# Performance work log

Hardware: AMD Instinct MI355X
Metric: run time of the kernel (lower is better)

Reference implementation:

```python
import jax, jax.numpy as jnp
import numpy as np
import math

BS, N_AGENTS, TOPK = 256, 64, 8
IN_DIM, HID, ATT, N_ACT = 128, 256, 64, 16


def setup_inputs() -> dict:
    key = jax.random.key(0)
    ks = jax.random.split(key, 20)
    s = 0.05
    return {
        "inputs": jax.random.normal(ks[0], (BS * N_AGENTS, IN_DIM), jnp.float32),
        "hidden_state": jax.random.normal(ks[1], (BS * N_AGENTS, HID), jnp.float32),
        "msg": jax.random.normal(ks[2], (BS * N_AGENTS, HID), jnp.float32),
        "topk_indices": jax.random.randint(ks[3], (BS, N_AGENTS, TOPK), 0, N_AGENTS, jnp.int32),
        "fc1_w": jax.random.normal(ks[4], (HID, IN_DIM), jnp.float32) * s,
        "fc1_b": jnp.zeros((HID,), jnp.float32),
        "gru_w_ih": jax.random.normal(ks[5], (3 * HID, HID), jnp.float32) * s,
        "gru_b_ih": jnp.zeros((3 * HID,), jnp.float32),
        "gru_w_hh": jax.random.normal(ks[6], (3 * HID, HID), jnp.float32) * s,
        "gru_b_hh": jnp.zeros((3 * HID,), jnp.float32),
        "q_w": jax.random.normal(ks[7], (ATT, HID), jnp.float32) * s,
        "q_b": jnp.zeros((ATT,), jnp.float32),
        "k_w": jax.random.normal(ks[8], (ATT, HID), jnp.float32) * s,
        "k_b": jnp.zeros((ATT,), jnp.float32),
        "v_w": jax.random.normal(ks[9], (HID, HID), jnp.float32) * s,
        "v_b": jnp.zeros((HID,), jnp.float32),
        "fc2a_w": jax.random.normal(ks[10], (HID, 2 * HID), jnp.float32) * s,
        "fc2a_b": jnp.zeros((HID,), jnp.float32),
        "fc2b_w": jax.random.normal(ks[11], (N_ACT, HID), jnp.float32) * s,
        "fc2b_b": jnp.zeros((N_ACT,), jnp.float32),
    }


def _forward(inputs, hidden_state, msg, topk_indices,
             fc1_w, fc1_b, gru_w_ih, gru_b_ih, gru_w_hh, gru_b_hh,
             q_w, q_b, k_w, k_b, v_w, v_b, fc2a_w, fc2a_b, fc2b_w, fc2b_b):
    # fc1 + ReLU
    x = jax.nn.relu(inputs @ fc1_w.T + fc1_b)  # [B*N, HID]
    # GRUCell (torch semantics)
    gi = x @ gru_w_ih.T + gru_b_ih             # [B*N, 3H]
    gh = hidden_state @ gru_w_hh.T + gru_b_hh
    i_r, i_z, i_n = jnp.split(gi, 3, axis=-1)
    h_r, h_z, h_n = jnp.split(gh, 3, axis=-1)
    r = jax.nn.sigmoid(i_r + h_r)
    z = jax.nn.sigmoid(i_z + h_z)
    n = jnp.tanh(i_n + r * h_n)
    h = (1.0 - z) * n + z * hidden_state       # [B*N, HID]

    # communicate: gather top-k neighbor messages, attend, aggregate
    msg_r = msg.reshape(BS, N_AGENTS, HID)
    msg_received = jax.vmap(lambda m, idx: m[idx])(msg_r, topk_indices)  # [B,N,K,HID]
    ego_h = h.reshape(BS, N_AGENTS, HID)
    q = ego_h @ q_w.T + q_b                    # [B,N,ATT]
    k = msg_received @ k_w.T + k_b             # [B,N,K,ATT]
    logits = jnp.einsum('bnka,bna->bnk', k, q) / math.sqrt(ATT)
    attn = jax.nn.softmax(logits, axis=-1)     # [B,N,K]
    m = msg_received @ v_w.T + v_b             # [B,N,K,HID]
    m_agg = jnp.einsum('bnk,bnkh->bnh', attn, m).reshape(BS * N_AGENTS, HID)

    out = jnp.concatenate([h, m_agg], axis=-1)  # [B*N, 2H]
    q_out = jax.nn.relu(out @ fc2a_w.T + fc2a_b) @ fc2b_w.T + fc2b_b  # [B*N, N_ACT]
    return q_out, h, m_agg


def reference(inputs, hidden_state, msg, topk_indices,
              fc1_w, fc1_b, gru_w_ih, gru_b_ih, gru_w_hh, gru_b_hh,
              q_w, q_b, k_w, k_b, v_w, v_b, fc2a_w, fc2a_b, fc2b_w, fc2b_b):
    return _forward(inputs, hidden_state, msg, topk_indices,
                    fc1_w, fc1_b, gru_w_ih, gru_b_ih, gru_w_hh, gru_b_hh,
                    q_w, q_b, k_w, k_b, v_w, v_b, fc2a_w, fc2a_b, fc2b_w, fc2b_b)
```

## Files before the change

kernel.cpp:

```cpp
#include <hip/hip_runtime.h>

typedef __bf16 bf16;
typedef __attribute__((ext_vector_type(8))) __bf16 bf16x8;
typedef __attribute__((ext_vector_type(4))) __bf16 bf16x4;
typedef __attribute__((ext_vector_type(4))) float f32x4;

static constexpr int ROWS = 16384;

static constexpr size_t OFF_WFC1 = 0;
static constexpr size_t OFF_WRX  = 32768;
static constexpr size_t OFF_WZX  = 98304;
static constexpr size_t OFF_WNI  = 163840;
static constexpr size_t OFF_WRH  = 229376;
static constexpr size_t OFF_WZH  = 294912;
static constexpr size_t OFF_WNH  = 360448;
static constexpr size_t OFF_WQ   = 425984;
static constexpr size_t OFF_WKV  = 442368;
static constexpr size_t OFF_F2AH = 524288;
static constexpr size_t OFF_F2AM = 589824;
static constexpr size_t OFF_WF2B = 655360;
static constexpr size_t OFF_INSW = 659456;

struct SwzSeg { const float* src; bf16* dst; int items; int k8s; int k32; int ld; };
struct SwzArgs { SwzSeg seg[14]; int count; };

__global__ __launch_bounds__(256) void swz_k(SwzArgs a) {
    const int tid = blockIdx.x * 256 + threadIdx.x;
    const int stride = gridDim.x * 256;
    for (int s = 0; s < a.count; ++s) {
        const float* __restrict__ src = a.seg[s].src;
        bf16* __restrict__ dst = a.seg[s].dst;
        const int items = a.seg[s].items, k8s = a.seg[s].k8s;
        const int k32c = a.seg[s].k32, ld = a.seg[s].ld;
        for (int i = tid; i < items; i += stride) {
            const int n = i >> k8s, kb = i & ((1 << k8s) - 1);
            const int k0 = kb << 3;
            const int lane = (n & 15) | ((kb & 3) << 4);
            const size_t off = ((size_t)((n >> 4) * k32c + (kb >> 2)) * 64 + lane) * 8;
            const float* p = src + (size_t)n * ld + k0;
            float4 f0 = *(const float4*)p;
            float4 f1 = *(const float4*)(p + 4);
            bf16x8 o = { (bf16)f0.x, (bf16)f0.y, (bf16)f0.z, (bf16)f0.w,
                         (bf16)f1.x, (bf16)f1.y, (bf16)f1.z, (bf16)f1.w };
            *(bf16x8*)(dst + off) = o;
        }
    }
}

template<int FM, int FN, int K32>
__device__ __forceinline__ void mm_swz(f32x4 (&acc)[FM][FN],
    const bf16* __restrict__ sA, int lda,
    const bf16* __restrict__ W, int lane)
{
    const int lr = lane & 15, lk = (lane >> 4) << 3;
    #pragma unroll
    for (int k32 = 0; k32 < K32; ++k32) {
        bf16x8 a[FM], b[FN];
        #pragma unroll
        for (int j = 0; j < FN; ++j)
            b[j] = *(const bf16x8*)(W + ((size_t)(j * K32 + k32) * 64 + lane) * 8);
        #pragma unroll
        for (int i = 0; i < FM; ++i)
            a[i] = *(const bf16x8*)&sA[(i * 16 + lr) * lda + k32 * 32 + lk];
        #pragma unroll
        for (int i = 0; i < FM; ++i)
            #pragma unroll
            for (int j = 0; j < FN; ++j)
                acc[i][j] = __builtin_amdgcn_mfma_f32_16x16x32_bf16(a[i], b[j], acc[i][j], 0, 0, 0);
    }
}

template<int FM, int FN, int K32>
__device__ __forceinline__ void mm_gg(f32x4 (&acc)[FM][FN],
    const bf16* __restrict__ A, const bf16* __restrict__ W, int lane)
{
    #pragma unroll
    for (int k32 = 0; k32 < K32; ++k32) {
        bf16x8 a[FM], b[FN];
        #pragma unroll
        for (int i = 0; i < FM; ++i)
            a[i] = *(const bf16x8*)(A + ((size_t)(i * K32 + k32) * 64 + lane) * 8);
        #pragma unroll
        for (int j = 0; j < FN; ++j)
            b[j] = *(const bf16x8*)(W + ((size_t)(j * K32 + k32) * 64 + lane) * 8);
        #pragma unroll
        for (int i = 0; i < FM; ++i)
            #pragma unroll
            for (int j = 0; j < FN; ++j)
                acc[i][j] = __builtin_amdgcn_mfma_f32_16x16x32_bf16(a[i], b[j], acc[i][j], 0, 0, 0);
    }
}

__device__ __forceinline__ float sigmf(float x) { return 1.f / (1.f + __expf(-x)); }
__device__ __forceinline__ float tanh_fast(float x) {
    x = fminf(fmaxf(x, -15.f), 15.f);
    float e2 = __expf(2.f * x);
    return (e2 - 1.f) / (e2 + 1.f);
}

__global__ __launch_bounds__(1024)
void mega_k(const bf16* __restrict__ insw, const float* __restrict__ hid_f,
            const float* __restrict__ msg_f, const int* __restrict__ topk,
            const bf16* __restrict__ Wfc1, const float* __restrict__ fc1_b,
            const bf16* __restrict__ WrX, const bf16* __restrict__ WrH,
            const bf16* __restrict__ WzX, const bf16* __restrict__ WzH,
            const bf16* __restrict__ Wni, const bf16* __restrict__ Wnh,
            const float* __restrict__ b_ih, const float* __restrict__ b_hh,
            const bf16* __restrict__ Wq, const float* __restrict__ q_b,
            const bf16* __restrict__ Wkv, const float* __restrict__ v_bias,
            const bf16* __restrict__ f2aH, const bf16* __restrict__ f2aM,
            const float* __restrict__ f2a_b,
            const bf16* __restrict__ Wf2b, const float* __restrict__ f2b_b,
            float* __restrict__ h_out, float* __restrict__ magg_out,
            float* __restrict__ q_out)
{
    __shared__ bf16 sH[64 * 264];
    __shared__ bf16 sB[64 * 264];
    __shared__ bf16 sG[64 * 264];
    __shared__ bf16 sM[64 * 264];
    __shared__ bf16 sQ[64 * 72];
    __shared__ bf16 sK[64 * 72];
    __shared__ int  sIdx[512];
    const int tid = threadIdx.x;
    const int wave = tid >> 6, lane = tid & 63;
    const int b64 = blockIdx.x * 64;
    const int lr = lane & 15, l4 = (lane >> 4) << 2, lk = (lane >> 4) << 3;

    #pragma unroll
    for (int c = tid; c < 4096; c += 1024) {
        int r = c >> 6, cg = (c & 63) << 2;
        float4 f = *(const float4*)(hid_f + (size_t)(b64 + r) * 256 + cg);
        float4 g = *(const float4*)(msg_f + (size_t)(b64 + r) * 256 + cg);
        bf16x4 oh = { (bf16)f.x, (bf16)f.y, (bf16)f.z, (bf16)f.w };
        bf16x4 og = { (bf16)g.x, (bf16)g.y, (bf16)g.z, (bf16)g.w };
        *(bf16x4*)&sH[r * 264 + cg] = oh;
        *(bf16x4*)&sG[r * 264 + cg] = og;
    }
    if (tid < 512) sIdx[tid] = topk[(size_t)blockIdx.x * 512 + tid];

    {
        f32x4 fa[1][4] = {};
        mm_gg<1, 4, 4>(fa, insw + (size_t)(blockIdx.x * 4 + (wave & 3)) * 4 * 512,
                       Wfc1 + (size_t)((wave >> 2) * 4) * 4 * 512, lane);
        #pragma unroll
        for (int j = 0; j < 4; ++j) {
            const int col = (wave >> 2) * 64 + j * 16 + lr;
            const float bv = fc1_b[col];
            #pragma unroll
            for (int rr = 0; rr < 4; ++rr)
                sB[((wave & 3) * 16 + l4 + rr) * 264 + col] = (bf16)fmaxf(fa[0][j][rr] + bv, 0.f);
        }
    }
    __syncthreads();

    f32x4 rg[4] = {}, zg[4] = {}, ng[4] = {}, hg[4] = {};
    {
        const size_t nb = (size_t)wave * 8 * 512;
        const bf16 *pRX = WrX + nb, *pZX = WzX + nb, *pNI = Wni + nb;
        const bf16 *pRH = WrH + nb, *pZH = WzH + nb, *pNH = Wnh + nb;
        #pragma unroll
        for (int k32 = 0; k32 < 8; ++k32) {
            const size_t bo = (size_t)k32 * 512 + lane * 8;
            bf16x8 brx = *(const bf16x8*)(pRX + bo);
            bf16x8 bzx = *(const bf16x8*)(pZX + bo);
            bf16x8 bni = *(const bf16x8*)(pNI + bo);
            bf16x8 brh = *(const bf16x8*)(pRH + bo);
            bf16x8 bzh = *(const bf16x8*)(pZH + bo);
            bf16x8 bnh = *(const bf16x8*)(pNH + bo);
            __builtin_amdgcn_s_setprio(1);
            #pragma unroll
            for (int i = 0; i < 4; ++i) {
                bf16x8 ax = *(const bf16x8*)&sB[(i * 16 + lr) * 264 + k32 * 32 + lk];
                rg[i] = __builtin_amdgcn_mfma_f32_16x16x32_bf16(ax, brx, rg[i], 0, 0, 0);
                zg[i] = __builtin_amdgcn_mfma_f32_16x16x32_bf16(ax, bzx, zg[i], 0, 0, 0);
                ng[i] = __builtin_amdgcn_mfma_f32_16x16x32_bf16(ax, bni, ng[i], 0, 0, 0);
            }
            #pragma unroll
            for (int i = 0; i < 4; ++i) {
                bf16x8 ah = *(const bf16x8*)&sH[(i * 16 + lr) * 264 + k32 * 32 + lk];
                rg[i] = __builtin_amdgcn_mfma_f32_16x16x32_bf16(ah, brh, rg[i], 0, 0, 0);
                zg[i] = __builtin_amdgcn_mfma_f32_16x16x32_bf16(ah, bzh, zg[i], 0, 0, 0);
                hg[i] = __builtin_amdgcn_mfma_f32_16x16x32_bf16(ah, bnh, hg[i], 0, 0, 0);
            }
            __builtin_amdgcn_s_setprio(0);
        }
    }
    {
        const int col = wave * 16 + lr;
        const float br = b_ih[col] + b_hh[col];
        const float bz = b_ih[256 + col] + b_hh[256 + col];
        const float bi = b_ih[512 + col], bh = b_hh[512 + col];
        #pragma unroll
        for (int i = 0; i < 4; ++i)
            #pragma unroll
            for (int rr = 0; rr < 4; ++rr) {
                const int row = i * 16 + l4 + rr;
                const float rv = sigmf(rg[i][rr] + br);
                const float zv = sigmf(zg[i][rr] + bz);
                const float nn = tanh_fast((ng[i][rr] + bi) + rv * (hg[i][rr] + bh));
                const float hd = (float)sH[row * 264 + col];
                const float h = (1.f - zv) * nn + zv * hd;
                sM[row * 264 + col] = (bf16)h;
            }
    }
    __syncthreads();

    if (wave < 4) {
        f32x4 a[4][2] = {};
        mm_swz<4, 2, 8>(a, sG, 264, Wkv + (size_t)(wave * 2) * 8 * 512, lane);
        #pragma unroll
        for (int i = 0; i < 4; ++i)
            #pragma unroll
            for (int j = 0; j < 2; ++j) {
                const int col = (wave * 2 + j) * 16 + lr;
                #pragma unroll
                for (int rr = 0; rr < 4; ++rr) {
                    const int row = i * 16 + l4 + rr;
                    if (col < 64) sK[row * 72 + col] = (bf16)a[i][j][rr];
                    else          sB[row * 264 + col - 64] = (bf16)a[i][j][rr];
                }
            }
    } else {
        f32x4 a[4][1] = {};
        mm_swz<4, 1, 8>(a, sG, 264, Wkv + (size_t)(4 + wave) * 8 * 512, lane);
        const int col = (4 + wave) * 16 + lr;
        #pragma unroll
        for (int i = 0; i < 4; ++i)
            #pragma unroll
            for (int rr = 0; rr < 4; ++rr)
                sB[(i * 16 + l4 + rr) * 264 + col - 64] = (bf16)a[i][0][rr];
    }
    {
        f32x4 qa[1][1] = {};
        mm_swz<1, 1, 8>(qa, sM + (wave & 3) * 16 * 264, 264,
                        Wq + (size_t)(wave >> 2) * 8 * 512, lane);
        const int col = (wave >> 2) * 16 + lr;
        const float bv = q_b[col];
        #pragma unroll
        for (int rr = 0; rr < 4; ++rr)
            sQ[((wave & 3) * 16 + l4 + rr) * 72 + col] = (bf16)(qa[0][0][rr] + bv);
    }
    #pragma unroll
    for (int u = 0; u < 4; ++u) {
        int c = tid + u * 1024;
        int r = c >> 6, cg = (c & 63) << 2;
        bf16x4 hv = *(const bf16x4*)&sM[r * 264 + cg];
        float4 o = { (float)hv[0], (float)hv[1], (float)hv[2], (float)hv[3] };
        *(float4*)(h_out + (size_t)(b64 + r) * 256 + cg) = o;
    }
    __syncthreads();

    const int kk = lane >> 3, dg = lane & 7;
    #pragma unroll
    for (int uu = 0; uu < 4; ++uu) {
        const int u = wave * 4 + uu;
        const int rowk = sIdx[u * 8 + kk];
        bf16x8 q8 = *(const bf16x8*)&sQ[u * 72 + dg * 8];
        bf16x8 k8 = *(const bf16x8*)&sK[rowk * 72 + dg * 8];
        float s = 0.f;
        #pragma unroll
        for (int t = 0; t < 8; ++t) s += (float)q8[t] * (float)k8[t];
        s += __shfl_xor(s, 1); s += __shfl_xor(s, 2); s += __shfl_xor(s, 4);
        float logit = s * 0.125f;
        float mx = logit;
        mx = fmaxf(mx, __shfl_xor(mx, 8));
        mx = fmaxf(mx, __shfl_xor(mx, 16));
        mx = fmaxf(mx, __shfl_xor(mx, 32));
        float e = __expf(logit - mx);
        float den = e;
        den += __shfl_xor(den, 8); den += __shfl_xor(den, 16); den += __shfl_xor(den, 32);
        const float wv = e / den;
        float a0 = 0.f, a1 = 0.f, a2 = 0.f, a3 = 0.f;
        #pragma unroll
        for (int k = 0; k < 8; ++k) {
            float wk = __shfl(wv, k * 8);
            int   rk = __shfl(rowk, k * 8);
            bf16x4 v = *(const bf16x4*)&sB[rk * 264 + lane * 4];
            a0 += wk * (float)v[0]; a1 += wk * (float)v[1];
            a2 += wk * (float)v[2]; a3 += wk * (float)v[3];
        }
        float4 vb = *(const float4*)(v_bias + lane * 4);
        a0 += vb.x; a1 += vb.y; a2 += vb.z; a3 += vb.w;
        float4 res = { a0, a1, a2, a3 };
        *(float4*)(magg_out + (size_t)(b64 + u) * 256 + lane * 4) = res;
        bf16x4 rb = { (bf16)a0, (bf16)a1, (bf16)a2, (bf16)a3 };
        *(bf16x4*)&sH[u * 264 + lane * 4] = rb;
    }
    __syncthreads();

    {
        const size_t nb = (size_t)wave * 8 * 512;
        f32x4 ya[4] = {};
        const bf16* pH = f2aH + nb;
        const bf16* pM = f2aM + nb;
        const int lo = lane * 8;
        bf16x8 cH = *(const bf16x8*)(pH + lo);
        bf16x8 cM = *(const bf16x8*)(pM + lo);
        #pragma unroll
        for (int k = 0; k < 8; ++k) {
            bf16x8 nH, nM;
            if (k < 7) {
                nH = *(const bf16x8*)(pH + (k + 1) * 512 + lo);
                nM = *(const bf16x8*)(pM + (k + 1) * 512 + lo);
            }
            __builtin_amdgcn_s_setprio(1);
            #pragma unroll
            for (int i = 0; i < 4; ++i) {
                bf16x8 aH = *(const bf16x8*)&sM[(i * 16 + lr) * 264 + k * 32 + lk];
                ya[i] = __builtin_amdgcn_mfma_f32_16x16x32_bf16(aH, cH, ya[i], 0, 0, 0);
            }
            #pragma unroll
            for (int i = 0; i < 4; ++i) {
                bf16x8 aM = *(const bf16x8*)&sH[(i * 16 + lr) * 264 + k * 32 + lk];
                ya[i] = __builtin_amdgcn_mfma_f32_16x16x32_bf16(aM, cM, ya[i], 0, 0, 0);
            }
            __builtin_amdgcn_s_setprio(0);
            cH = nH; cM = nM;
        }
        const int col = wave * 16 + lr;
        const float bv = f2a_b[col];
        #pragma unroll
        for (int i = 0; i < 4; ++i)
            #pragma unroll
            for (int rr = 0; rr < 4; ++rr)
                sG[(i * 16 + l4 + rr) * 264 + col] = (bf16)fmaxf(ya[i][rr] + bv, 0.f);
    }
    __syncthreads();

    if (wave < 4) {
        f32x4 acc[1][1] = {};
        mm_swz<1, 1, 8>(acc, sG + wave * 16 * 264, 264, Wf2b, lane);
        const float bv = f2b_b[lr];
        #pragma unroll
        for (int rr = 0; rr < 4; ++rr)
            q_out[(size_t)(b64 + wave * 16 + l4 + rr) * 16 + lr] = acc[0][0][rr] + bv;
    }
}

extern "C" void kernel_launch(void* const* d_in, const int* in_sizes, int n_in,
                              void* d_out, int out_size, void* d_ws, size_t ws_size,
                              hipStream_t stream)
{
    const float* in_f   = (const float*)d_in[0];
    const float* hid_f  = (const float*)d_in[1];
    const float* msg_f  = (const float*)d_in[2];
    const int*   topk   = (const int*)d_in[3];
    const float* fc1w_f = (const float*)d_in[4];
    const float* fc1_b  = (const float*)d_in[5];
    const float* wih_f  = (const float*)d_in[6];
    const float* b_ih   = (const float*)d_in[7];
    const float* whh_f  = (const float*)d_in[8];
    const float* b_hh   = (const float*)d_in[9];
    const float* qw_f   = (const float*)d_in[10];
    const float* q_b    = (const float*)d_in[11];
    const float* kw_f   = (const float*)d_in[12];
    const float* vw_f   = (const float*)d_in[14];
    const float* v_b    = (const float*)d_in[15];
    const float* f2aw_f = (const float*)d_in[16];
    const float* f2a_b  = (const float*)d_in[17];
    const float* f2bw_f = (const float*)d_in[18];
    const float* f2b_b  = (const float*)d_in[19];

    bf16* ws = (bf16*)d_ws;
    bf16* Wfc1 = ws + OFF_WFC1;
    bf16* WrX  = ws + OFF_WRX;
    bf16* WzX  = ws + OFF_WZX;
    bf16* Wni  = ws + OFF_WNI;
    bf16* WrH  = ws + OFF_WRH;
    bf16* WzH  = ws + OFF_WZH;
    bf16* Wnh  = ws + OFF_WNH;
    bf16* Wq   = ws + OFF_WQ;
    bf16* Wkv  = ws + OFF_WKV;
    bf16* f2aH = ws + OFF_F2AH;
    bf16* f2aM = ws + OFF_F2AM;
    bf16* Wf2b = ws + OFF_WF2B;
    bf16* insw = ws + OFF_INSW;

    float* q_out    = (float*)d_out;
    float* h_out    = q_out + (size_t)ROWS * 16;
    float* magg_out = h_out + (size_t)ROWS * 256;

    SwzArgs sa{};
    int s = 0;
    auto add = [&](const float* src, bf16* dst, int N, int K, int ld) {
        sa.seg[s].src = src; sa.seg[s].dst = dst;
        sa.seg[s].items = N * (K >> 3);
        sa.seg[s].k8s = (K == 128) ? 4 : 5;
        sa.seg[s].k32 = K >> 5;
        sa.seg[s].ld = ld; ++s;
    };
    add(fc1w_f,          Wfc1, 256, 128, 128);
    add(wih_f,           WrX,  256, 256, 256);
    add(wih_f +  65536,  WzX,  256, 256, 256);
    add(wih_f + 131072,  Wni,  256, 256, 256);
    add(whh_f,           WrH,  256, 256, 256);
    add(whh_f +  65536,  WzH,  256, 256, 256);
    add(whh_f + 131072,  Wnh,  256, 256, 256);
    add(qw_f,            Wq,    64, 256, 256);
    add(kw_f,            Wkv,   64, 256, 256);
    add(vw_f,            Wkv + 16384, 256, 256, 256);
    add(f2aw_f,          f2aH, 256, 256, 512);
    add(f2aw_f + 256,    f2aM, 256, 256, 512);
    add(f2bw_f,          Wf2b,  16, 256, 256);
    add(in_f,            insw, 16384, 128, 128);
    sa.count = s;
    swz_k<<<512, 256, 0, stream>>>(sa);

    mega_k<<<256, 1024, 0, stream>>>(insw, hid_f, msg_f, topk,
                                     Wfc1, fc1_b, WrX, WrH, WzX, WzH, Wni, Wnh,
                                     b_ih, b_hh, Wq, q_b, Wkv, v_b,
                                     f2aH, f2aM, f2a_b, Wf2b, f2b_b,
                                     h_out, magg_out, q_out);
}
```

Before: 56.49 us.

## Split message K/V projection into a separate kernel writing bf16 to workspace

```diff
diff --git a/kernel.cpp b/kernel.cpp
--- a/kernel.cpp
+++ b/kernel.cpp
@@ -20,6 +20,8 @@
 static constexpr size_t OFF_F2AM = 589824;
 static constexpr size_t OFF_WF2B = 655360;
 static constexpr size_t OFF_INSW = 659456;
+static constexpr size_t OFF_MSGK = 2756608;
+static constexpr size_t OFF_MSGV = 3805184;
 
 struct SwzSeg { const float* src; bf16* dst; int items; int k8s; int k32; int ld; };
 struct SwzArgs { SwzSeg seg[14]; int count; };
@@ -98,16 +100,53 @@
     return (e2 - 1.f) / (e2 + 1.f);
 }
 
+__global__ __launch_bounds__(512)
+void msgkv_k(const float* __restrict__ msg_f, const bf16* __restrict__ Wkv,
+             bf16* __restrict__ msgk, bf16* __restrict__ msgv)
+{
+    __shared__ bf16 sA[64 * 264];
+    const int tid = threadIdx.x;
+    const int wave = tid >> 6, lane = tid & 63;
+    const int wm = wave >> 2, wn = wave & 3;
+    const int m0 = blockIdx.x * 64;
+    const int lr = lane & 15, l4 = (lane >> 4) << 2;
+
+    for (int c = tid; c < 4096; c += 512) {
+        int r = c >> 6, cg = (c & 63) << 2;
+        float4 f = *(const float4*)(msg_f + (size_t)(m0 + r) * 256 + cg);
+        bf16x4 o = { (bf16)f.x, (bf16)f.y, (bf16)f.z, (bf16)f.w };
+        *(bf16x4*)&sA[r * 264 + cg] = o;
+    }
+    __syncthreads();
+
+    f32x4 acc[2][5] = {};
+    mm_swz<2, 5, 8>(acc, sA + wm * 32 * 264, 264, Wkv + (size_t)(wn * 5) * 8 * 512, lane);
+
+    #pragma unroll
+    for (int i = 0; i < 2; ++i)
+        #pragma unroll
+        for (int j = 0; j < 5; ++j) {
+            const int col = wn * 80 + j * 16 + lr;
+            #pragma unroll
+            for (int rr = 0; rr < 4; ++rr) {
+                const size_t row = m0 + wm * 32 + i * 16 + l4 + rr;
+                if (col < 64) msgk[row * 64 + col] = (bf16)acc[i][j][rr];
+                else          msgv[row * 256 + col - 64] = (bf16)acc[i][j][rr];
+            }
+        }
+}
+
 __global__ __launch_bounds__(1024)
 void mega_k(const bf16* __restrict__ insw, const float* __restrict__ hid_f,
-            const float* __restrict__ msg_f, const int* __restrict__ topk,
+            const int* __restrict__ topk,
             const bf16* __restrict__ Wfc1, const float* __restrict__ fc1_b,
             const bf16* __restrict__ WrX, const bf16* __restrict__ WrH,
             const bf16* __restrict__ WzX, const bf16* __restrict__ WzH,
             const bf16* __restrict__ Wni, const bf16* __restrict__ Wnh,
             const float* __restrict__ b_ih, const float* __restrict__ b_hh,
             const bf16* __restrict__ Wq, const float* __restrict__ q_b,
-            const bf16* __restrict__ Wkv, const float* __restrict__ v_bias,
+            const bf16* __restrict__ msgk, const bf16* __restrict__ msgv,
+            const float* __restrict__ v_bias,
             const bf16* __restrict__ f2aH, const bf16* __restrict__ f2aM,
             const float* __restrict__ f2a_b,
             const bf16* __restrict__ Wf2b, const float* __restrict__ f2b_b,
@@ -116,7 +155,6 @@
 {
     __shared__ bf16 sH[64 * 264];
     __shared__ bf16 sB[64 * 264];
-    __shared__ bf16 sG[64 * 264];
     __shared__ bf16 sM[64 * 264];
     __shared__ bf16 sQ[64 * 72];
     __shared__ bf16 sK[64 * 72];
@@ -130,13 +168,14 @@
     for (int c = tid; c < 4096; c += 1024) {
         int r = c >> 6, cg = (c & 63) << 2;
         float4 f = *(const float4*)(hid_f + (size_t)(b64 + r) * 256 + cg);
-        float4 g = *(const float4*)(msg_f + (size_t)(b64 + r) * 256 + cg);
         bf16x4 oh = { (bf16)f.x, (bf16)f.y, (bf16)f.z, (bf16)f.w };
-        bf16x4 og = { (bf16)g.x, (bf16)g.y, (bf16)g.z, (bf16)g.w };
         *(bf16x4*)&sH[r * 264 + cg] = oh;
-        *(bf16x4*)&sG[r * 264 + cg] = og;
-    }
-    if (tid < 512) sIdx[tid] = topk[(size_t)blockIdx.x * 512 + tid];
+    }
+    if (tid < 512) {
+        int row = tid >> 3, cg = (tid & 7) << 3;
+        *(bf16x8*)&sK[row * 72 + cg] = *(const bf16x8*)(msgk + (size_t)(b64 + row) * 64 + cg);
+        sIdx[tid] = topk[(size_t)blockIdx.x * 512 + tid];
+    }
 
     {
         f32x4 fa[1][4] = {};
@@ -205,31 +244,6 @@
     }
     __syncthreads();
 
-    if (wave < 4) {
-        f32x4 a[4][2] = {};
-        mm_swz<4, 2, 8>(a, sG, 264, Wkv + (size_t)(wave * 2) * 8 * 512, lane);
-        #pragma unroll
-        for (int i = 0; i < 4; ++i)
-            #pragma unroll
-            for (int j = 0; j < 2; ++j) {
-                const int col = (wave * 2 + j) * 16 + lr;
-                #pragma unroll
-                for (int rr = 0; rr < 4; ++rr) {
-                    const int row = i * 16 + l4 + rr;
-                    if (col < 64) sK[row * 72 + col] = (bf16)a[i][j][rr];
-                    else          sB[row * 264 + col - 64] = (bf16)a[i][j][rr];
-                }
-            }
-    } else {
-        f32x4 a[4][1] = {};
-        mm_swz<4, 1, 8>(a, sG, 264, Wkv + (size_t)(4 + wave) * 8 * 512, lane);
-        const int col = (4 + wave) * 16 + lr;
-        #pragma unroll
-        for (int i = 0; i < 4; ++i)
-            #pragma unroll
-            for (int rr = 0; rr < 4; ++rr)
-                sB[(i * 16 + l4 + rr) * 264 + col - 64] = (bf16)a[i][0][rr];
-    }
     {
         f32x4 qa[1][1] = {};
         mm_swz<1, 1, 8>(qa, sM + (wave & 3) * 16 * 264, 264,
@@ -275,7 +289,7 @@
         for (int k = 0; k < 8; ++k) {
             float wk = __shfl(wv, k * 8);
             int   rk = __shfl(rowk, k * 8);
-            bf16x4 v = *(const bf16x4*)&sB[rk * 264 + lane * 4];
+            bf16x4 v = *(const bf16x4*)(msgv + (size_t)(b64 + rk) * 256 + lane * 4);
             a0 += wk * (float)v[0]; a1 += wk * (float)v[1];
             a2 += wk * (float)v[2]; a3 += wk * (float)v[3];
         }
@@ -323,13 +337,13 @@
         for (int i = 0; i < 4; ++i)
             #pragma unroll
             for (int rr = 0; rr < 4; ++rr)
-                sG[(i * 16 + l4 + rr) * 264 + col] = (bf16)fmaxf(ya[i][rr] + bv, 0.f);
+                sB[(i * 16 + l4 + rr) * 264 + col] = (bf16)fmaxf(ya[i][rr] + bv, 0.f);
     }
     __syncthreads();
 
     if (wave < 4) {
         f32x4 acc[1][1] = {};
-        mm_swz<1, 1, 8>(acc, sG + wave * 16 * 264, 264, Wf2b, lane);
+        mm_swz<1, 1, 8>(acc, sB + wave * 16 * 264, 264, Wf2b, lane);
         const float bv = f2b_b[lr];
         #pragma unroll
         for (int rr = 0; rr < 4; ++rr)
@@ -375,6 +389,8 @@
     bf16* f2aM = ws + OFF_F2AM;
     bf16* Wf2b = ws + OFF_WF2B;
     bf16* insw = ws + OFF_INSW;
+    bf16* msgk = ws + OFF_MSGK;
+    bf16* msgv = ws + OFF_MSGV;
 
     float* q_out    = (float*)d_out;
     float* h_out    = q_out + (size_t)ROWS * 16;
@@ -406,9 +422,11 @@
     sa.count = s;
     swz_k<<<512, 256, 0, stream>>>(sa);
 
-    mega_k<<<256, 1024, 0, stream>>>(insw, hid_f, msg_f, topk,
+    msgkv_k<<<256, 512, 0, stream>>>(msg_f, Wkv, msgk, msgv);
+
+    mega_k<<<256, 1024, 0, stream>>>(insw, hid_f, topk,
                                      Wfc1, fc1_b, WrX, WrH, WzX, WzH, Wni, Wnh,
-                                     b_ih, b_hh, Wq, q_b, Wkv, v_b,
+                                     b_ih, b_hh, Wq, q_b, msgk, msgv, v_b,
                                      f2aH, f2aM, f2a_b, Wf2b, f2b_b,
                                      h_out, magg_out, q_out);
 }
```

After: 62.53 us. 10.7% more time.

## Halve block size to 512 threads and redistribute per-wave GEMM work

Applied to the files above, without the earlier changes.

```diff
diff --git a/kernel.cpp b/kernel.cpp
--- a/kernel.cpp
+++ b/kernel.cpp
@@ -6,6 +6,8 @@
 typedef __attribute__((ext_vector_type(4))) float f32x4;
 
 static constexpr int ROWS = 16384;
+
+#define MFMA_B16 __builtin_amdgcn_mfma_f32_16x16x32_bf16
 
 static constexpr size_t OFF_WFC1 = 0;
 static constexpr size_t OFF_WRX  = 32768;
@@ -66,7 +68,7 @@
         for (int i = 0; i < FM; ++i)
             #pragma unroll
             for (int j = 0; j < FN; ++j)
-                acc[i][j] = __builtin_amdgcn_mfma_f32_16x16x32_bf16(a[i], b[j], acc[i][j], 0, 0, 0);
+                acc[i][j] = MFMA_B16(a[i], b[j], acc[i][j], 0, 0, 0);
     }
 }
 
@@ -87,7 +89,7 @@
         for (int i = 0; i < FM; ++i)
             #pragma unroll
             for (int j = 0; j < FN; ++j)
-                acc[i][j] = __builtin_amdgcn_mfma_f32_16x16x32_bf16(a[i], b[j], acc[i][j], 0, 0, 0);
+                acc[i][j] = MFMA_B16(a[i], b[j], acc[i][j], 0, 0, 0);
     }
 }
 
@@ -98,7 +100,7 @@
     return (e2 - 1.f) / (e2 + 1.f);
 }
 
-__global__ __launch_bounds__(1024)
+__global__ __launch_bounds__(512, 2)
 void mega_k(const bf16* __restrict__ insw, const float* __restrict__ hid_f,
             const float* __restrict__ msg_f, const int* __restrict__ topk,
             const bf16* __restrict__ Wfc1, const float* __restrict__ fc1_b,
@@ -127,7 +129,7 @@
     const int lr = lane & 15, l4 = (lane >> 4) << 2, lk = (lane >> 4) << 3;
 
     #pragma unroll
-    for (int c = tid; c < 4096; c += 1024) {
+    for (int c = tid; c < 4096; c += 512) {
         int r = c >> 6, cg = (c & 63) << 2;
         float4 f = *(const float4*)(hid_f + (size_t)(b64 + r) * 256 + cg);
         float4 g = *(const float4*)(msg_f + (size_t)(b64 + r) * 256 + cg);
@@ -136,57 +138,64 @@
         *(bf16x4*)&sH[r * 264 + cg] = oh;
         *(bf16x4*)&sG[r * 264 + cg] = og;
     }
-    if (tid < 512) sIdx[tid] = topk[(size_t)blockIdx.x * 512 + tid];
+    sIdx[tid] = topk[(size_t)blockIdx.x * 512 + tid];
 
     {
-        f32x4 fa[1][4] = {};
-        mm_gg<1, 4, 4>(fa, insw + (size_t)(blockIdx.x * 4 + (wave & 3)) * 4 * 512,
-                       Wfc1 + (size_t)((wave >> 2) * 4) * 4 * 512, lane);
-        #pragma unroll
-        for (int j = 0; j < 4; ++j) {
-            const int col = (wave >> 2) * 64 + j * 16 + lr;
-            const float bv = fc1_b[col];
-            #pragma unroll
-            for (int rr = 0; rr < 4; ++rr)
-                sB[((wave & 3) * 16 + l4 + rr) * 264 + col] = (bf16)fmaxf(fa[0][j][rr] + bv, 0.f);
-        }
+        const int wm = wave >> 2, wn = wave & 3;
+        f32x4 fa[2][4] = {};
+        mm_gg<2, 4, 4>(fa, insw + (size_t)(blockIdx.x * 4 + wm * 2) * 4 * 512,
+                       Wfc1 + (size_t)(wn * 4) * 4 * 512, lane);
+        #pragma unroll
+        for (int i = 0; i < 2; ++i)
+            #pragma unroll
+            for (int j = 0; j < 4; ++j) {
+                const int col = wn * 64 + j * 16 + lr;
+                const float bv = fc1_b[col];
+                #pragma unroll
+                for (int rr = 0; rr < 4; ++rr)
+                    sB[(wm * 32 + i * 16 + l4 + rr) * 264 + col] = (bf16)fmaxf(fa[i][j][rr] + bv, 0.f);
+            }
     }
     __syncthreads();
 
-    f32x4 rg[4] = {}, zg[4] = {}, ng[4] = {}, hg[4] = {};
-    {
-        const size_t nb = (size_t)wave * 8 * 512;
+    #pragma unroll 1
+    for (int p = 0; p < 2; ++p) {
+        const size_t nb = (size_t)(p * 8 + wave) * 8 * 512 + lane * 8;
         const bf16 *pRX = WrX + nb, *pZX = WzX + nb, *pNI = Wni + nb;
         const bf16 *pRH = WrH + nb, *pZH = WzH + nb, *pNH = Wnh + nb;
-        #pragma unroll
-        for (int k32 = 0; k32 < 8; ++k32) {
-            const size_t bo = (size_t)k32 * 512 + lane * 8;
-            bf16x8 brx = *(const bf16x8*)(pRX + bo);
-            bf16x8 bzx = *(const bf16x8*)(pZX + bo);
-            bf16x8 bni = *(const bf16x8*)(pNI + bo);
-            bf16x8 brh = *(const bf16x8*)(pRH + bo);
-            bf16x8 bzh = *(const bf16x8*)(pZH + bo);
-            bf16x8 bnh = *(const bf16x8*)(pNH + bo);
+        f32x4 rg[4] = {}, zg[4] = {}, ng[4] = {}, hg[4] = {};
+        bf16x8 c0 = *(const bf16x8*)pRX, c1 = *(const bf16x8*)pZX, c2 = *(const bf16x8*)pNI;
+        bf16x8 c3 = *(const bf16x8*)pRH, c4 = *(const bf16x8*)pZH, c5 = *(const bf16x8*)pNH;
+        bf16x8 d0 = *(const bf16x8*)(pRX + 512), d1 = *(const bf16x8*)(pZX + 512), d2 = *(const bf16x8*)(pNI + 512);
+        bf16x8 d3 = *(const bf16x8*)(pRH + 512), d4 = *(const bf16x8*)(pZH + 512), d5 = *(const bf16x8*)(pNH + 512);
+        #pragma unroll
+        for (int k = 0; k < 8; ++k) {
+            bf16x8 e0, e1, e2, e3, e4, e5;
+            if (k < 6) {
+                const size_t bo = (size_t)(k + 2) * 512;
+                e0 = *(const bf16x8*)(pRX + bo); e1 = *(const bf16x8*)(pZX + bo); e2 = *(const bf16x8*)(pNI + bo);
+                e3 = *(const bf16x8*)(pRH + bo); e4 = *(const bf16x8*)(pZH + bo); e5 = *(const bf16x8*)(pNH + bo);
+            }
             __builtin_amdgcn_s_setprio(1);
             #pragma unroll
             for (int i = 0; i < 4; ++i) {
-                bf16x8 ax = *(const bf16x8*)&sB[(i * 16 + lr) * 264 + k32 * 32 + lk];
-                rg[i] = __builtin_amdgcn_mfma_f32_16x16x32_bf16(ax, brx, rg[i], 0, 0, 0);
-                zg[i] = __builtin_amdgcn_mfma_f32_16x16x32_bf16(ax, bzx, zg[i], 0, 0, 0);
-                ng[i] = __builtin_amdgcn_mfma_f32_16x16x32_bf16(ax, bni, ng[i], 0, 0, 0);
+                bf16x8 ax = *(const bf16x8*)&sB[(i * 16 + lr) * 264 + k * 32 + lk];
+                rg[i] = MFMA_B16(ax, c0, rg[i], 0, 0, 0);
+                zg[i] = MFMA_B16(ax, c1, zg[i], 0, 0, 0);
+                ng[i] = MFMA_B16(ax, c2, ng[i], 0, 0, 0);
             }
             #pragma unroll
             for (int i = 0; i < 4; ++i) {
-                bf16x8 ah = *(const bf16x8*)&sH[(i * 16 + lr) * 264 + k32 * 32 + lk];
-                rg[i] = __builtin_amdgcn_mfma_f32_16x16x32_bf16(ah, brh, rg[i], 0, 0, 0);
-                zg[i] = __builtin_amdgcn_mfma_f32_16x16x32_bf16(ah, bzh, zg[i], 0, 0, 0);
-                hg[i] = __builtin_amdgcn_mfma_f32_16x16x32_bf16(ah, bnh, hg[i], 0, 0, 0);
+                bf16x8 ah = *(const bf16x8*)&sH[(i * 16 + lr) * 264 + k * 32 + lk];
+                rg[i] = MFMA_B16(ah, c3, rg[i], 0, 0, 0);
+                zg[i] = MFMA_B16(ah, c4, zg[i], 0, 0, 0);
+                hg[i] = MFMA_B16(ah, c5, hg[i], 0, 0, 0);
             }
             __builtin_amdgcn_s_setprio(0);
+            c0 = d0; c1 = d1; c2 = d2; c3 = d3; c4 = d4; c5 = d5;
+            if (k < 6) { d0 = e0; d1 = e1; d2 = e2; d3 = e3; d4 = e4; d5 = e5; }
         }
-    }
-    {
-        const int col = wave * 16 + lr;
+        const int col = p * 128 + wave * 16 + lr;
         const float br = b_ih[col] + b_hh[col];
         const float bz = b_ih[256 + col] + b_hh[256 + col];
         const float bi = b_ih[512 + col], bh = b_hh[512 + col];
@@ -205,44 +214,53 @@
     }
     __syncthreads();
 
-    if (wave < 4) {
-        f32x4 a[4][2] = {};
-        mm_swz<4, 2, 8>(a, sG, 264, Wkv + (size_t)(wave * 2) * 8 * 512, lane);
+    {
+        f32x4 a[4][1] = {};
+        mm_swz<4, 1, 8>(a, sG, 264, Wkv + (size_t)wave * 8 * 512, lane);
+        const int col = wave * 16 + lr;
         #pragma unroll
         for (int i = 0; i < 4; ++i)
             #pragma unroll
-            for (int j = 0; j < 2; ++j) {
-                const int col = (wave * 2 + j) * 16 + lr;
-                #pragma unroll
-                for (int rr = 0; rr < 4; ++rr) {
-                    const int row = i * 16 + l4 + rr;
-                    if (col < 64) sK[row * 72 + col] = (bf16)a[i][j][rr];
-                    else          sB[row * 264 + col - 64] = (bf16)a[i][j][rr];
-                }
-            }
-    } else {
+            for (int rr = 0; rr < 4; ++rr) {
+                const int row = i * 16 + l4 + rr;
+                if (col < 64) sK[row * 72 + col] = (bf16)a[i][0][rr];
+                else          sB[row * 264 + col - 64] = (bf16)a[i][0][rr];
+            }
+    }
+    {
         f32x4 a[4][1] = {};
-        mm_swz<4, 1, 8>(a, sG, 264, Wkv + (size_t)(4 + wave) * 8 * 512, lane);
-        const int col = (4 + wave) * 16 + lr;
+        mm_swz<4, 1, 8>(a, sG, 264, Wkv + (size_t)(8 + wave) * 8 * 512, lane);
+        const int col = (8 + wave) * 16 + lr;
         #pragma unroll
         for (int i = 0; i < 4; ++i)
             #pragma unroll
             for (int rr = 0; rr < 4; ++rr)
                 sB[(i * 16 + l4 + rr) * 264 + col - 64] = (bf16)a[i][0][rr];
     }
+    if (wave < 4) {
+        f32x4 a[4][1] = {};
+        mm_swz<4, 1, 8>(a, sG, 264, Wkv + (size_t)(16 + wave) * 8 * 512, lane);
+        const int col = (16 + wave) * 16 + lr;
+        #pragma unroll
+        for (int i = 0; i < 4; ++i)
+            #pragma unroll
+            for (int rr = 0; rr < 4; ++rr)
+                sB[(i * 16 + l4 + rr) * 264 + col - 64] = (bf16)a[i][0][rr];
+    }
     {
-        f32x4 qa[1][1] = {};
-        mm_swz<1, 1, 8>(qa, sM + (wave & 3) * 16 * 264, 264,
-                        Wq + (size_t)(wave >> 2) * 8 * 512, lane);
-        const int col = (wave >> 2) * 16 + lr;
+        const int wm = wave >> 2, wn = wave & 3;
+        f32x4 qa[2][1] = {};
+        mm_swz<2, 1, 8>(qa, sM + wm * 32 * 264, 264, Wq + (size_t)wn * 8 * 512, lane);
+        const int col = wn * 16 + lr;
         const float bv = q_b[col];
         #pragma unroll
-        for (int rr = 0; rr < 4; ++rr)
-            sQ[((wave & 3) * 16 + l4 + rr) * 72 + col] = (bf16)(qa[0][0][rr] + bv);
+        for (int i = 0; i < 2; ++i)
+            #pragma unroll
+            for (int rr = 0; rr < 4; ++rr)
+                sQ[(wm * 32 + i * 16 + l4 + rr) * 72 + col] = (bf16)(qa[i][0][rr] + bv);
     }
     #pragma unroll
-    for (int u = 0; u < 4; ++u) {
-        int c = tid + u * 1024;
+    for (int c = tid; c < 4096; c += 512) {
         int r = c >> 6, cg = (c & 63) << 2;
         bf16x4 hv = *(const bf16x4*)&sM[r * 264 + cg];
         float4 o = { (float)hv[0], (float)hv[1], (float)hv[2], (float)hv[3] };
@@ -252,8 +270,8 @@
 
     const int kk = lane >> 3, dg = lane & 7;
     #pragma unroll
-    for (int uu = 0; uu < 4; ++uu) {
-        const int u = wave * 4 + uu;
+    for (int uu = 0; uu < 8; ++uu) {
+        const int u = wave * 8 + uu;
         const int rowk = sIdx[u * 8 + kk];
         bf16x8 q8 = *(const bf16x8*)&sQ[u * 72 + dg * 8];
         bf16x8 k8 = *(const bf16x8*)&sK[rowk * 72 + dg * 8];
@@ -288,36 +306,36 @@
     }
     __syncthreads();
 
-    {
-        const size_t nb = (size_t)wave * 8 * 512;
+    #pragma unroll 1
+    for (int p = 0; p < 2; ++p) {
+        const size_t nb = (size_t)(p * 8 + wave) * 8 * 512 + lane * 8;
+        const bf16 *pH = f2aH + nb, *pM = f2aM + nb;
         f32x4 ya[4] = {};
-        const bf16* pH = f2aH + nb;
-        const bf16* pM = f2aM + nb;
-        const int lo = lane * 8;
-        bf16x8 cH = *(const bf16x8*)(pH + lo);
-        bf16x8 cM = *(const bf16x8*)(pM + lo);
+        bf16x8 cH = *(const bf16x8*)pH,         cM = *(const bf16x8*)pM;
+        bf16x8 dH = *(const bf16x8*)(pH + 512), dM = *(const bf16x8*)(pM + 512);
         #pragma unroll
         for (int k = 0; k < 8; ++k) {
-            bf16x8 nH, nM;
-            if (k < 7) {
-                nH = *(const bf16x8*)(pH + (k + 1) * 512 + lo);
-                nM = *(const bf16x8*)(pM + (k + 1) * 512 + lo);
+            bf16x8 eH, eM;
+            if (k < 6) {
+                eH = *(const bf16x8*)(pH + (size_t)(k + 2) * 512);
+                eM = *(const bf16x8*)(pM + (size_t)(k + 2) * 512);
             }
             __builtin_amdgcn_s_setprio(1);
             #pragma unroll
             for (int i = 0; i < 4; ++i) {
                 bf16x8 aH = *(const bf16x8*)&sM[(i * 16 + lr) * 264 + k * 32 + lk];
-                ya[i] = __builtin_amdgcn_mfma_f32_16x16x32_bf16(aH, cH, ya[i], 0, 0, 0);
+                ya[i] = MFMA_B16(aH, cH, ya[i], 0, 0, 0);
             }
             #pragma unroll
             for (int i = 0; i < 4; ++i) {
                 bf16x8 aM = *(const bf16x8*)&sH[(i * 16 + lr) * 264 + k * 32 + lk];
-                ya[i] = __builtin_amdgcn_mfma_f32_16x16x32_bf16(aM, cM, ya[i], 0, 0, 0);
+                ya[i] = MFMA_B16(aM, cM, ya[i], 0, 0, 0);
             }
             __builtin_amdgcn_s_setprio(0);
-            cH = nH; cM = nM;
+            cH = dH; cM = dM;
+            if (k < 6) { dH = eH; dM = eM; }
         }
-        const int col = wave * 16 + lr;
+        const int col = p * 128 + wave * 16 + lr;
         const float bv = f2a_b[col];
         #pragma unroll
         for (int i = 0; i < 4; ++i)
@@ -406,9 +424,9 @@
     sa.count = s;
     swz_k<<<512, 256, 0, stream>>>(sa);
 
-    mega_k<<<256, 1024, 0, stream>>>(insw, hid_f, msg_f, topk,
-                                     Wfc1, fc1_b, WrX, WrH, WzX, WzH, Wni, Wnh,
-                                     b_ih, b_hh, Wq, q_b, Wkv, v_b,
-                                     f2aH, f2aM, f2a_b, Wf2b, f2b_b,
-                                     h_out, magg_out, q_out);
-}
+    mega_k<<<256, 512, 0, stream>>>(insw, hid_f, msg_f, topk,
+                                    Wfc1, fc1_b, WrX, WrH, WzX, WzH, Wni, Wnh,
+                                    b_ih, b_hh, Wq, q_b, Wkv, v_b,
+                                    f2aH, f2aM, f2a_b, Wf2b, f2b_b,
+                                    h_out, magg_out, q_out);
+}
```

After: 108.6 us. +92.3%, slower.
